# Kernel tuning notes

Measured on AMD Instinct MI355X. Metric: run time of the kernel, lower is better.

Reference implementation:

```python
import jax, jax.numpy as jnp
import numpy as np

# Model dims (ViT-Base @ 384)
L, H, D, HD, M, P, IMG, B, NC, CH = 12, 12, 768, 64, 3072, 16, 384, 32, 1000, 3
NPATCH = (IMG // P) ** 2  # 576
SCALE = 1.0 / np.sqrt(HD)


def setup_inputs() -> dict:
    key = jax.random.key(0)
    ks = iter(jax.random.split(key, 16))
    def n(shape, s=0.02):
        return (jax.random.normal(next(ks), shape, jnp.float32) * s).astype(jnp.float32)
    return dict(
        x=jax.random.normal(next(ks), (B, CH, IMG, IMG), jnp.float32),
        conv_w=n((D, CH, P, P)), conv_b=jnp.zeros((D,), jnp.float32),
        cls_token=jnp.zeros((1, 1, D), jnp.float32),
        pos_emb=n((1, NPATCH + 1, D), 1.0),
        ln1_g=jnp.ones((L, D), jnp.float32), ln1_b=jnp.zeros((L, D), jnp.float32),
        wqkv=n((L, H, D, 3 * HD)), bqkv=jnp.zeros((L, H, 3 * HD), jnp.float32),
        wmsa=n((L, D, D)), bmsa=jnp.zeros((L, D), jnp.float32),
        ln2_g=jnp.ones((L, D), jnp.float32), ln2_b=jnp.zeros((L, D), jnp.float32),
        lnm_g=jnp.ones((L, D), jnp.float32), lnm_b=jnp.zeros((L, D), jnp.float32),
        w1=n((L, D, M)), b1=jnp.zeros((L, M), jnp.float32),
        w2=n((L, M, D)), b2=jnp.zeros((L, D), jnp.float32),
        lnf_g=jnp.ones((D,), jnp.float32), lnf_b=jnp.zeros((D,), jnp.float32),
        whead=n((D, NC)), bhead=jnp.zeros((NC,), jnp.float32),
    )


def _ln(x, g, b, eps=1e-5):
    mu = jnp.mean(x, axis=-1, keepdims=True)
    var = jnp.mean(jnp.square(x - mu), axis=-1, keepdims=True)
    return (x - mu) * jax.lax.rsqrt(var + eps) * g + b


def _encoder_block(x, p):
    (ln1_g, ln1_b, wqkv, bqkv, wmsa, bmsa,
     ln2_g, ln2_b, lnm_g, lnm_b, w1, b1, w2, b2) = p
    b = x.shape[0]
    h = _ln(x, ln1_g, ln1_b)
    # batched per-head QKV (math identical to looping over H small Linears)
    qkv = jnp.einsum('bsd,hde->bhse', h, wqkv) + bqkv[:, None, :]  # [B,H,S,3*HD]
    q, k, v = jnp.split(qkv, 3, axis=-1)
    attn = jax.nn.softmax(jnp.einsum('bhqe,bhke->bhqk', q, k) * SCALE, axis=-1)
    o = jnp.einsum('bhqk,bhke->bhqe', attn, v)          # [B,H,S,HD]
    o = o.transpose(0, 2, 1, 3).reshape(b, -1, D)        # concat heads along feature
    msa = jnp.einsum('bsd,de->bse', o, wmsa) + bmsa
    x1 = h + msa                                          # residual around MSA (post-LN1)
    h2 = _ln(x1, ln2_g, ln2_b)
    h2 = _ln(h2, lnm_g, lnm_b)                            # MLPBlock's own LayerNorm (double LN, faithful)
    mlp = jnp.einsum('bsm,md->bsd', jax.nn.gelu(jnp.einsum('bsd,dm->bsm', h2, w1) + b1, approximate=False), w2) + b2
    return x1 + mlp, None


def reference(x, conv_w, conv_b, cls_token, pos_emb,
              ln1_g, ln1_b, wqkv, bqkv, wmsa, bmsa,
              ln2_g, ln2_b, lnm_g, lnm_b, w1, b1, w2, b2,
              lnf_g, lnf_b, whead, bhead):
    b = x.shape[0]
    # patchify conv (image divisible by patch, so F.pad is a no-op)
    t = jax.lax.conv_general_dilated(x, conv_w, (P, P), 'VALID',
                                     dimension_numbers=('NCHW', 'OIHW', 'NCHW'))
    t = t + conv_b[None, :, None, None]
    # faithful to torch .view(b, -1, embed_dim) on NCHW layout (channel-major flatten)
    t = t.reshape(b, -1, D)
    n = t.shape[1]
    t = jnp.concatenate([jnp.broadcast_to(cls_token, (b, 1, D)), t], axis=1)
    t = t + pos_emb[:, :n + 1]
    stacked = (ln1_g, ln1_b, wqkv, bqkv, wmsa, bmsa,
               ln2_g, ln2_b, lnm_g, lnm_b, w1, b1, w2, b2)
    t, _ = jax.lax.scan(_encoder_block, t, stacked)
    y = _ln(t[:, 0], lnf_g, lnf_b)
    y = jax.nn.softmax(jnp.einsum('bd,dc->bc', y, whead) + bhead, axis=-1)
    return y
```

## Files before the change

### kernel.cpp

```cpp
#include <hip/hip_runtime.h>

using f16   = _Float16;
using f16x8 = __attribute__((ext_vector_type(8))) _Float16;
using f32x4 = __attribute__((ext_vector_type(4))) float;

#define MPAD  18560
#define MREAL 18464
#define MCONV 18432
#define SEQ   577
#define SPAD  640
#define NHEAD 12
#define NBATCH 32
#define SC2   0.18033688f
#define THR2  11.5416f

__device__ __forceinline__ void load_lds16(const void* g, void* l) {
  __builtin_amdgcn_global_load_lds(
      (const __attribute__((address_space(1))) void*)g,
      (__attribute__((address_space(3))) void*)l, 16, 0, 0);
}

template<int K, int EPI>
__global__ __launch_bounds__(256) void gemm_k(
    const f16* __restrict__ A, const f16* __restrict__ Bt,
    const float* __restrict__ bias, const float* __restrict__ res,
    float* __restrict__ o32, f16* __restrict__ o16a, f16* __restrict__ o16b,
    f16* __restrict__ o16c, const float* __restrict__ pos,
    const float* __restrict__ lng, const float* __restrict__ lnb,
    const float* __restrict__ stats, int N, int Mreal)
{
  static_assert(K % 64 == 0, "BK=64");
  __shared__ __align__(16) f16 As[128 * 64];
  __shared__ __align__(16) f16 Bs[128 * 64];
  const int tid = threadIdx.x;
  const int lane = tid & 63, wv = tid >> 6;

  const int gx = gridDim.x, gy = gridDim.y;
  const int nwg = gx * gy;
  const int flat = blockIdx.y * gx + blockIdx.x;
  const int xcd = flat & 7;
  const int qq = nwg >> 3, rr = nwg & 7;
  const int p_ = ((xcd < rr) ? xcd * (qq + 1) : rr * (qq + 1) + (xcd - rr) * qq)
                 + (flat >> 3);
  const int bandsz = gy * 6;
  const int band = p_ / bandsz, within = p_ - band * bandsz;
  const int byi = within / 6;
  const int bxi = band * 6 + (within - byi * 6);
  const int bm = byi << 7, bn = bxi << 7;

  const int wm = (wv >> 1) << 6, wn = (wv & 1) << 6;
  const int r16 = lane & 15, g4 = lane >> 4;
  const f32x4 Z4 = {0.f, 0.f, 0.f, 0.f};

  f32x4 acc[4][4];
#pragma unroll
  for (int m = 0; m < 4; ++m)
#pragma unroll
    for (int n = 0; n < 4; ++n) acc[m][n] = Z4;

  const int srow = lane >> 3;
  const int sgc  = (lane & 7) ^ srow;
  const f16* Agp = A  + (size_t)(bm + srow) * K + sgc * 8;
  const f16* Bgp = Bt + (size_t)(bn + srow) * K + sgc * 8;

  for (int k0 = 0; k0 < K; k0 += 64) {
#pragma unroll
    for (int j = 0; j < 4; ++j) {
      const size_t roff = (size_t)((wv * 4 + j) * 8) * K + k0;
      load_lds16(Agp + roff, As + (wv * 4 + j) * 512);
      load_lds16(Bgp + roff, Bs + (wv * 4 + j) * 512);
    }
    __syncthreads();
#pragma unroll
    for (int ks = 0; ks < 2; ++ks) {
      f16x8 af[4], bf[4];
#pragma unroll
      for (int m = 0; m < 4; ++m) {
        int row = wm + m * 16 + r16;
        af[m] = *(const f16x8*)(As + row * 64 + ((((ks << 2) | g4) ^ (row & 7)) << 3));
      }
#pragma unroll
      for (int n = 0; n < 4; ++n) {
        int row = wn + n * 16 + r16;
        bf[n] = *(const f16x8*)(Bs + row * 64 + ((((ks << 2) | g4) ^ (row & 7)) << 3));
      }
#pragma unroll
      for (int m = 0; m < 4; ++m)
#pragma unroll
        for (int n = 0; n < 4; ++n)
          acc[m][n] = __builtin_amdgcn_mfma_f32_16x16x32_f16(af[m], bf[n], acc[m][n], 0, 0, 0);
    }
    __syncthreads();
  }

#pragma unroll
  for (int m = 0; m < 4; ++m) {
#pragma unroll
    for (int n = 0; n < 4; ++n) {
#pragma unroll
      for (int r = 0; r < 4; ++r) {
        int grow = bm + wm + m * 16 + g4 * 4 + r;
        int gcol = bn + wn + n * 16 + r16;
        float v = acc[m][n][r];
        if constexpr (EPI == 0) {
          if (grow < Mreal) {
            int b = grow / 576, p = grow - b * 576;
            int i = gcol * 576 + p;
            int sp = i / 768, dd = i - sp * 768;
            o32[((size_t)(b * SEQ + sp + 1)) * 768 + dd] =
                v + bias[gcol] + pos[(size_t)(sp + 1) * 768 + dd];
          }
        } else if constexpr (EPI == 1) {
          if (grow < Mreal) {
            int b = grow / SEQ, s = grow - b * SEQ;
            int hq = gcol / 192, rem = gcol - hq * 192;
            int sel = rem >> 6, e = rem & 63;
            float val = v + bias[gcol];
            int bh = b * NHEAD + hq;
            if (sel == 0)      o16a[((size_t)bh * SPAD + s) * 64 + e] = (f16)val;
            else if (sel == 1) o16b[((size_t)bh * SPAD + s) * 64 + e] = (f16)val;
            else               o16c[((size_t)bh * 64 + e) * SPAD + s] = (f16)val;
          }
        } else if constexpr (EPI == 2) {
          size_t idx = (size_t)grow * N + gcol;
          o32[idx] = v + bias[gcol] + res[idx];
        } else if constexpr (EPI == 4) {
          if (grow < Mreal) {
            size_t idx = (size_t)grow * N + gcol;
            float mu = stats[2 * grow], rs = stats[2 * grow + 1];
            float h = (res[idx] - mu) * rs * lng[gcol] + lnb[gcol];
            o32[idx] = v + bias[gcol] + h;
          }
        } else {
          float val = v + bias[gcol];
          float gl = 0.5f * val * (1.0f + erff(val * 0.70710678f));
          o16a[(size_t)grow * N + gcol] = (f16)gl;
        }
      }
    }
  }
}

__device__ __forceinline__ void block_red2(float& a, float& b, float* sm, int tid) {
  __syncthreads();
#pragma unroll
  for (int d = 32; d; d >>= 1) { a += __shfl_down(a, d); b += __shfl_down(b, d); }
  if ((tid & 63) == 0) { int w = tid >> 6; sm[w] = a; sm[w + 4] = b; }
  __syncthreads();
  a = sm[0] + sm[1] + sm[2] + sm[3];
  b = sm[4] + sm[5] + sm[6] + sm[7];
}

__global__ __launch_bounds__(256) void ln_fwd(const float* __restrict__ X,
    const float* __restrict__ g, const float* __restrict__ bb,
    float* __restrict__ stats, f16* __restrict__ hh)
{
  int row = blockIdx.x, tid = threadIdx.x;
  const float* x = X + (size_t)row * 768;
  float v0 = x[tid], v1 = x[tid + 256], v2 = x[tid + 512];
  float s = v0 + v1 + v2, s2 = v0*v0 + v1*v1 + v2*v2;
  __shared__ float sm[8];
  block_red2(s, s2, sm, tid);
  float mu = s * (1.f/768.f);
  float var = s2 * (1.f/768.f) - mu * mu;
  float rs = rsqrtf(var + 1e-5f);
  if (tid == 0) { stats[2 * row] = mu; stats[2 * row + 1] = rs; }
  size_t base = (size_t)row * 768;
  hh[base + tid      ] = (f16)((v0 - mu) * rs * g[tid      ] + bb[tid      ]);
  hh[base + tid + 256] = (f16)((v1 - mu) * rs * g[tid + 256] + bb[tid + 256]);
  hh[base + tid + 512] = (f16)((v2 - mu) * rs * g[tid + 512] + bb[tid + 512]);
}

__global__ __launch_bounds__(256) void ln2_fwd(const float* __restrict__ X,
    const float* __restrict__ g2, const float* __restrict__ bb2,
    const float* __restrict__ gm, const float* __restrict__ bbm,
    f16* __restrict__ hh)
{
  int row = blockIdx.x, tid = threadIdx.x;
  const float* x = X + (size_t)row * 768;
  float v0 = x[tid], v1 = x[tid + 256], v2 = x[tid + 512];
  float s = v0 + v1 + v2, s2 = v0*v0 + v1*v1 + v2*v2;
  __shared__ float sm[8];
  block_red2(s, s2, sm, tid);
  float mu = s * (1.f/768.f), var = s2 * (1.f/768.f) - mu * mu;
  float rs = rsqrtf(var + 1e-5f);
  float y0 = (v0 - mu) * rs * g2[tid      ] + bb2[tid      ];
  float y1 = (v1 - mu) * rs * g2[tid + 256] + bb2[tid + 256];
  float y2 = (v2 - mu) * rs * g2[tid + 512] + bb2[tid + 512];
  s = y0 + y1 + y2; s2 = y0*y0 + y1*y1 + y2*y2;
  block_red2(s, s2, sm, tid);
  mu = s * (1.f/768.f); var = s2 * (1.f/768.f) - mu * mu;
  rs = rsqrtf(var + 1e-5f);
  size_t base = (size_t)row * 768;
  hh[base + tid      ] = (f16)((y0 - mu) * rs * gm[tid      ] + bbm[tid      ]);
  hh[base + tid + 256] = (f16)((y1 - mu) * rs * gm[tid + 256] + bbm[tid + 256]);
  hh[base + tid + 512] = (f16)((y2 - mu) * rs * gm[tid + 512] + bbm[tid + 512]);
}

__global__ __launch_bounds__(256) void attn_k(const f16* __restrict__ qbuf,
    const f16* __restrict__ kbuf, const f16* __restrict__ vtbuf,
    f16* __restrict__ obuf)
{
  const int gx = gridDim.x;
  const int nwg = gx * gridDim.y;
  const int flat = blockIdx.y * gx + blockIdx.x;
  const int xcd = flat & 7;
  const int qq = nwg >> 3, rr = nwg & 7;
  const int pos_ = ((xcd < rr) ? xcd * (qq + 1) : rr * (qq + 1) + (xcd - rr) * qq)
                   + (flat >> 3);
  const int bh = pos_ / gx;
  const int s0 = (pos_ - bh * gx) << 6;

  const int b = bh / NHEAD, hd = bh - b * NHEAD;
  const int tid = threadIdx.x, lane = tid & 63, wv = tid >> 6;
  const int r16 = lane & 15, g4 = lane >> 4;
  const f16* Q  = qbuf  + (size_t)bh * SPAD * 64;
  const f16* Kg = kbuf  + (size_t)bh * SPAD * 64;
  const f16* Vg = vtbuf + (size_t)bh * 64 * SPAD;
  __shared__ __align__(16) f16 Kt[64 * 64];
  __shared__ __align__(16) f16 Vt[64 * 64];
  __shared__ __align__(16) f16 Pw[4][16][72];
  const f32x4 Z4 = {0.f, 0.f, 0.f, 0.f};

  f16x8 qf[2];
  {
    const f16* qr = Q + (size_t)(s0 + wv * 16 + r16) * 64;
    qf[0] = *(const f16x8*)(qr + g4 * 8);
    qf[1] = *(const f16x8*)(qr + 32 + g4 * 8);
  }
  float m_run[4] = {-1e30f, -1e30f, -1e30f, -1e30f};
  float l_part[4] = {0.f, 0.f, 0.f, 0.f};
  f32x4 o_acc[4];
#pragma unroll
  for (int n = 0; n < 4; ++n) o_acc[n] = Z4;

  auto tile = [&](int kt, bool mask) {
#pragma unroll
    for (int j = 0; j < 2; ++j) {
      int off = (wv * 2 + j) * 1024 + lane * 16;
      int row = off >> 7;
      int cs  = (off >> 4) & 7;
      int gc  = cs ^ (row & 7);
      load_lds16(Kg + (size_t)(kt + row) * 64 + gc * 8, (void*)((char*)Kt + (wv*2 + j) * 1024));
      load_lds16(Vg + (size_t)row * SPAD + kt + gc * 8, (void*)((char*)Vt + (wv*2 + j) * 1024));
    }
    __syncthreads();

    f32x4 sa[4];
#pragma unroll
    for (int n = 0; n < 4; ++n) sa[n] = Z4;
#pragma unroll
    for (int n = 0; n < 4; ++n) {
      int krow = n * 16 + r16;
#pragma unroll
      for (int kc = 0; kc < 2; ++kc) {
        f16x8 kf = *(const f16x8*)(Kt + krow * 64 + (((kc * 4 + g4) ^ (krow & 7)) << 3));
        sa[n] = __builtin_amdgcn_mfma_f32_16x16x32_f16(qf[kc], kf, sa[n], 0, 0, 0);
      }
    }
#pragma unroll
    for (int r = 0; r < 4; ++r) {
      float mx = -1e30f;
#pragma unroll
      for (int n = 0; n < 4; ++n) {
        float sv = sa[n][r] * SC2;
        if (mask && (kt + n * 16 + r16 >= SEQ)) sv = -1e30f;
        sa[n][r] = sv;
        mx = fmaxf(mx, sv);
      }
#pragma unroll
      for (int d = 1; d < 16; d <<= 1) mx = fmaxf(mx, __shfl_xor(mx, d));
      if (!__all(mx - m_run[r] <= THR2)) {
        float mnew = fmaxf(m_run[r], mx);
        float alpha = exp2f(m_run[r] - mnew);
        m_run[r] = mnew;
        l_part[r] *= alpha;
#pragma unroll
        for (int n = 0; n < 4; ++n) o_acc[n][r] *= alpha;
      }
#pragma unroll
      for (int n = 0; n < 4; ++n) {
        float p = exp2f(sa[n][r] - m_run[r]);
        l_part[r] += p;
        Pw[wv][g4 * 4 + r][n * 16 + r16] = (f16)p;
      }
    }
    f16x8 pf[2];
    pf[0] = *(const f16x8*)(&Pw[wv][r16][g4 * 8]);
    pf[1] = *(const f16x8*)(&Pw[wv][r16][32 + g4 * 8]);
#pragma unroll
    for (int n = 0; n < 4; ++n) {
      int erow = n * 16 + r16;
#pragma unroll
      for (int kc = 0; kc < 2; ++kc) {
        f16x8 vf = *(const f16x8*)(Vt + erow * 64 + (((kc * 4 + g4) ^ (erow & 7)) << 3));
        o_acc[n] = __builtin_amdgcn_mfma_f32_16x16x32_f16(pf[kc], vf, o_acc[n], 0, 0, 0);
      }
    }
    __syncthreads();
  };

#pragma unroll 1
  for (int kt = 0; kt < 576; kt += 64) tile(kt, false);
  tile(576, true);

  float inv[4];
#pragma unroll
  for (int r = 0; r < 4; ++r) {
    float l = l_part[r];
#pragma unroll
    for (int d = 1; d < 16; d <<= 1) l += __shfl_xor(l, d);
    inv[r] = 1.f / l;
  }
#pragma unroll
  for (int n = 0; n < 4; ++n)
#pragma unroll
    for (int r = 0; r < 4; ++r) {
      int s = s0 + wv * 16 + g4 * 4 + r;
      if (s < SEQ)
        obuf[((size_t)(b * SEQ + s)) * 768 + hd * 64 + n * 16 + r16] =
            (f16)(o_acc[n][r] * inv[r]);
    }
}

__global__ __launch_bounds__(256) void cvt_transpose(const float* __restrict__ in,
    f16* __restrict__ out, int K, int N, size_t ls_in, size_t ls_out)
{
  in  += (size_t)blockIdx.z * ls_in;
  out += (size_t)blockIdx.z * ls_out;
  __shared__ float t[32][33];
  int n0 = blockIdx.x << 5, k0 = blockIdx.y << 5;
  int tx = threadIdx.x & 31, ty = threadIdx.x >> 5;
#pragma unroll
  for (int i = 0; i < 4; ++i) t[ty + 8*i][tx] = in[(size_t)(k0 + ty + 8*i) * N + n0 + tx];
  __syncthreads();
#pragma unroll
  for (int i = 0; i < 4; ++i) out[(size_t)(n0 + ty + 8*i) * K + k0 + tx] = (f16)t[tx][ty + 8*i];
}

__global__ __launch_bounds__(256) void cvt_qkvw(const float* __restrict__ in,
    f16* __restrict__ out, size_t ls_in, size_t ls_out)
{
  in  += (size_t)blockIdx.z * ls_in;
  out += (size_t)blockIdx.z * ls_out;
  __shared__ float t[32][33];
  int n0 = blockIdx.x << 5, k0 = blockIdx.y << 5;
  int tx = threadIdx.x & 31, ty = threadIdx.x >> 5;
  int hq = n0 / 192, r0 = n0 - hq * 192;
#pragma unroll
  for (int i = 0; i < 4; ++i)
    t[ty + 8*i][tx] = in[(size_t)hq * 147456 + (size_t)(k0 + ty + 8*i) * 192 + r0 + tx];
  __syncthreads();
#pragma unroll
  for (int i = 0; i < 4; ++i) out[(size_t)(n0 + ty + 8*i) * 768 + k0 + tx] = (f16)t[tx][ty + 8*i];
}

__global__ __launch_bounds__(256) void cvt_plain(const float* __restrict__ in,
    f16* __restrict__ out, int n)
{
  int i = blockIdx.x * 1024 + threadIdx.x;
#pragma unroll
  for (int j = 0; j < 4; ++j) { int idx = i + j * 256; if (idx < n) out[idx] = (f16)in[idx]; }
}

__global__ __launch_bounds__(256) void zero_vpad(f16* __restrict__ vtb) {
  int bh = blockIdx.x;
  for (int idx = threadIdx.x; idx < 64 * (SPAD - SEQ); idx += 256) {
    int e = idx / (SPAD - SEQ), s = SEQ + idx - e * (SPAD - SEQ);
    vtb[((size_t)bh * 64 + e) * SPAD + s] = (f16)0.f;
  }
}

__global__ __launch_bounds__(256) void im2col_k(const float* __restrict__ x, f16* __restrict__ out) {
  int row = blockIdx.x;
  int b = row / 576, p = row - b * 576;
  int py = p / 24, px = p - py * 24;
  int tid = threadIdx.x;
#pragma unroll
  for (int j = 0; j < 3; ++j) {
    int k = tid + j * 256;
    int c = k >> 8, rem = k & 255;
    int iy = rem >> 4, ix = rem & 15;
    out[(size_t)row * 768 + k] =
        (f16)x[(((size_t)(b * 3 + c)) * 384 + py * 16 + iy) * 384 + px * 16 + ix];
  }
}

__global__ __launch_bounds__(256) void cls_k(const float* __restrict__ ct,
    const float* __restrict__ pos, float* __restrict__ X)
{
  int b = blockIdx.x, tid = threadIdx.x;
#pragma unroll
  for (int j = 0; j < 3; ++j) {
    int d0 = tid + j * 256;
    X[((size_t)b * SEQ) * 768 + d0] = ct[d0] + pos[d0];
  }
}

__global__ __launch_bounds__(256) void head_logits(const float* __restrict__ X,
    const float* __restrict__ g, const float* __restrict__ bb,
    const float* __restrict__ W, const float* __restrict__ bhd,
    float* __restrict__ lg)
{
  int b = blockIdx.x, tid = threadIdx.x;
  const float* x = X + (size_t)(b * SEQ) * 768;
  float v0 = x[tid], v1 = x[tid + 256], v2 = x[tid + 512];
  float s = v0 + v1 + v2, s2 = v0*v0 + v1*v1 + v2*v2;
  __shared__ float sm[8];
  block_red2(s, s2, sm, tid);
  float mu = s * (1.f/768.f), var = s2 * (1.f/768.f) - mu * mu;
  float rs = rsqrtf(var + 1e-5f);
  __shared__ float y[768];
  y[tid      ] = (v0 - mu) * rs * g[tid      ] + bb[tid      ];
  y[tid + 256] = (v1 - mu) * rs * g[tid + 256] + bb[tid + 256];
  y[tid + 512] = (v2 - mu) * rs * g[tid + 512] + bb[tid + 512];
  __syncthreads();
  int c = blockIdx.y * 250 + tid;
  if (tid < 250) {
    float a0 = 0.f, a1 = 0.f, a2 = 0.f, a3 = 0.f;
#pragma unroll 4
    for (int d = 0; d < 768; d += 4) {
      a0 = fmaf(y[d    ], W[(size_t)(d    ) * 1000 + c], a0);
      a1 = fmaf(y[d + 1], W[(size_t)(d + 1) * 1000 + c], a1);
      a2 = fmaf(y[d + 2], W[(size_t)(d + 2) * 1000 + c], a2);
      a3 = fmaf(y[d + 3], W[(size_t)(d + 3) * 1000 + c], a3);
    }
    lg[(size_t)b * 1000 + c] = (a0 + a1) + (a2 + a3) + bhd[c];
  }
}

__global__ __launch_bounds__(256) void head_soft(const float* __restrict__ lg,
    float* __restrict__ out)
{
  int b = blockIdx.x, tid = threadIdx.x;
  __shared__ float sm[8];
  float v[4], mx = -1e30f;
#pragma unroll
  for (int j = 0; j < 4; ++j) {
    int c = tid + j * 256;
    v[j] = (c < 1000) ? lg[(size_t)b * 1000 + c] : -1e30f;
    mx = fmaxf(mx, v[j]);
  }
#pragma unroll
  for (int d = 32; d; d >>= 1) mx = fmaxf(mx, __shfl_down(mx, d));
  if ((tid & 63) == 0) sm[tid >> 6] = mx;
  __syncthreads();
  mx = fmaxf(fmaxf(sm[0], sm[1]), fmaxf(sm[2], sm[3]));
  float se = 0.f, ex[4];
#pragma unroll
  for (int j = 0; j < 4; ++j) {
    int c = tid + j * 256;
    ex[j] = (c < 1000) ? __expf(v[j] - mx) : 0.f;
    se += ex[j];
  }
  __syncthreads();
#pragma unroll
  for (int d = 32; d; d >>= 1) se += __shfl_down(se, d);
  if ((tid & 63) == 0) sm[tid >> 6] = se;
  __syncthreads();
  se = sm[0] + sm[1] + sm[2] + sm[3];
  float inv = 1.f / se;
#pragma unroll
  for (int j = 0; j < 4; ++j) {
    int c = tid + j * 256;
    if (c < 1000) out[(size_t)b * 1000 + c] = ex[j] * inv;
  }
}

extern "C" void kernel_launch(void* const* d_in, const int* in_sizes, int n_in,
                              void* d_out, int out_size, void* d_ws, size_t ws_size,
                              hipStream_t stream)
{
  (void)in_sizes; (void)n_in; (void)out_size;
  const float* x      = (const float*)d_in[0];
  const float* conv_w = (const float*)d_in[1];
  const float* conv_b = (const float*)d_in[2];
  const float* cls_t  = (const float*)d_in[3];
  const float* pos    = (const float*)d_in[4];
  const float* ln1_g  = (const float*)d_in[5];
  const float* ln1_b  = (const float*)d_in[6];
  const float* wqkv   = (const float*)d_in[7];
  const float* bqkv   = (const float*)d_in[8];
  const float* wmsa   = (const float*)d_in[9];
  const float* bmsa   = (const float*)d_in[10];
  const float* ln2_g  = (const float*)d_in[11];
  const float* ln2_b  = (const float*)d_in[12];
  const float* lnm_g  = (const float*)d_in[13];
  const float* lnm_b  = (const float*)d_in[14];
  const float* w1     = (const float*)d_in[15];
  const float* b1     = (const float*)d_in[16];
  const float* w2     = (const float*)d_in[17];
  const float* b2     = (const float*)d_in[18];
  const float* lnf_g  = (const float*)d_in[19];
  const float* lnf_b  = (const float*)d_in[20];
  const float* whead  = (const float*)d_in[21];
  const float* bhead  = (const float*)d_in[22];
  float* out = (float*)d_out;

  const size_t szQ  = (size_t)2304 * 768;
  const size_t szM  = (size_t)768 * 768;
  const size_t szW1 = (size_t)3072 * 768;
  const size_t szW2 = (size_t)768 * 3072;
  const size_t fixed_bytes =
      (size_t)MPAD * 768 * 4 + (size_t)MPAD * 8 + 32 * 1000 * 4 +
      (size_t)MPAD * 768 * 2 +
      (size_t)MPAD * 3072 * 2 + 3 * ((size_t)NBATCH * NHEAD * SPAD * 64 * 2) +
      (size_t)768 * 768 * 2  + 16 * 256 ;
  const bool hoist =
      ws_size >= fixed_bytes + 12 * (szQ + szM + szW1 + szW2) * 2 + 8 * 256;
  const int LW = hoist ? 12 : 1;

  char* wsp = (char*)d_ws;
  size_t off = 0;
  auto alloc = [&](size_t bytes) {
    char* p = wsp + off; off += (bytes + 255) & ~(size_t)255; return p;
  };
  float* X    = (float*)alloc((size_t)MPAD * 768 * 4);
  float* stats= (float*)alloc((size_t)MPAD * 8);
  float* lgbuf= (float*)alloc((size_t)32 * 1000 * 4);
  f16*   hh   = (f16*)  alloc((size_t)MPAD * 768 * 2);
  f16*   abuf = (f16*)  alloc((size_t)MPAD * 3072 * 2);
  f16*   qb   = (f16*)  alloc((size_t)NBATCH * NHEAD * SPAD * 64 * 2);
  f16*   kb   = (f16*)  alloc((size_t)NBATCH * NHEAD * SPAD * 64 * 2);
  f16*   vtb  = (f16*)  alloc((size_t)NBATCH * NHEAD * SPAD * 64 * 2);
  f16*   WcT  = (f16*)  alloc((size_t)768 * 768 * 2);
  f16*   WqkvT= (f16*)  alloc(LW * szQ  * 2);
  f16*   WmsaT= (f16*)  alloc(LW * szM  * 2);
  f16*   W1T  = (f16*)  alloc(LW * szW1 * 2);
  f16*   W2T  = (f16*)  alloc(LW * szW2 * 2);
  f16*   obuf   = abuf;
  f16*   patchA = abuf;
  f16*   h2h    = hh;
  if (ws_size < off) return;

  zero_vpad<<<dim3(NBATCH * NHEAD), 256, 0, stream>>>(vtb);
  cvt_plain<<<dim3((768 * 768 + 1023) / 1024), 256, 0, stream>>>(conv_w, WcT, 768 * 768);
  if (hoist) {
    cvt_qkvw<<<dim3(72, 24, 12), 256, 0, stream>>>(wqkv, WqkvT, (size_t)12*768*192, szQ);
    cvt_transpose<<<dim3(24, 24, 12), 256, 0, stream>>>(wmsa, WmsaT, 768, 768, szM, szM);
    cvt_transpose<<<dim3(96, 24, 12), 256, 0, stream>>>(w1, W1T, 768, 3072, szW1, szW1);
    cvt_transpose<<<dim3(24, 96, 12), 256, 0, stream>>>(w2, W2T, 3072, 768, szW2, szW2);
  }
  im2col_k<<<dim3(MCONV), 256, 0, stream>>>(x, patchA);
  gemm_k<768, 0><<<dim3(6, 144), 256, 0, stream>>>(
      patchA, WcT, conv_b, nullptr, X, nullptr, nullptr, nullptr, pos,
      nullptr, nullptr, nullptr, 768, MCONV);
  cls_k<<<dim3(NBATCH), 256, 0, stream>>>(cls_t, pos, X);

  for (int l = 0; l < 12; ++l) {
    f16* wq  = WqkvT + (hoist ? (size_t)l * szQ  : 0);
    f16* wms = WmsaT + (hoist ? (size_t)l * szM  : 0);
    f16* w1t = W1T   + (hoist ? (size_t)l * szW1 : 0);
    f16* w2t = W2T   + (hoist ? (size_t)l * szW2 : 0);
    if (!hoist) {
      cvt_qkvw<<<dim3(72, 24), 256, 0, stream>>>(
          wqkv + (size_t)l * 12 * 768 * 192, wq, 0, 0);
      cvt_transpose<<<dim3(24, 24), 256, 0, stream>>>(
          wmsa + (size_t)l * 768 * 768, wms, 768, 768, 0, 0);
      cvt_transpose<<<dim3(96, 24), 256, 0, stream>>>(
          w1 + (size_t)l * 768 * 3072, w1t, 768, 3072, 0, 0);
      cvt_transpose<<<dim3(24, 96), 256, 0, stream>>>(
          w2 + (size_t)l * 3072 * 768, w2t, 3072, 768, 0, 0);
    }

    ln_fwd<<<dim3(MREAL), 256, 0, stream>>>(X, ln1_g + l * 768, ln1_b + l * 768, stats, hh);
    gemm_k<768, 1><<<dim3(18, 145), 256, 0, stream>>>(
        hh, wq, bqkv + (size_t)l * 2304, nullptr, nullptr, qb, kb, vtb, nullptr,
        nullptr, nullptr, nullptr, 2304, MREAL);
    attn_k<<<dim3(10, NBATCH * NHEAD), 256, 0, stream>>>(qb, kb, vtb, obuf);
    gemm_k<768, 4><<<dim3(6, 145), 256, 0, stream>>>(
        obuf, wms, bmsa + l * 768, X, X, nullptr, nullptr, nullptr, nullptr,
        ln1_g + l * 768, ln1_b + l * 768, stats, 768, MREAL);
    ln2_fwd<<<dim3(MREAL), 256, 0, stream>>>(
        X, ln2_g + l * 768, ln2_b + l * 768, lnm_g + l * 768, lnm_b + l * 768, h2h);
    gemm_k<768, 3><<<dim3(24, 145), 256, 0, stream>>>(
        h2h, w1t, b1 + (size_t)l * 3072, nullptr, nullptr, abuf, nullptr, nullptr, nullptr,
        nullptr, nullptr, nullptr, 3072, MREAL);
    gemm_k<3072, 2><<<dim3(6, 145), 256, 0, stream>>>(
        abuf, w2t, b2 + l * 768, X, X, nullptr, nullptr, nullptr, nullptr,
        nullptr, nullptr, nullptr, 768, MREAL);
  }
  head_logits<<<dim3(NBATCH, 4), 256, 0, stream>>>(X, lnf_g, lnf_b, whead, bhead, lgbuf);
  head_soft<<<dim3(NBATCH), 256, 0, stream>>>(lgbuf, out);
}
```

Before: 7.831 ms.

## Process two query tiles per attention block and hoist GEMM LDS offsets

```diff
diff --git a/kernel.cpp b/kernel.cpp
--- a/kernel.cpp
+++ b/kernel.cpp
@@ -63,6 +63,19 @@
   const f16* Agp = A  + (size_t)(bm + srow) * K + sgc * 8;
   const f16* Bgp = Bt + (size_t)(bn + srow) * K + sgc * 8;
 
+  int aoff[2][4], boff[2][4];
+#pragma unroll
+  for (int ks = 0; ks < 2; ++ks) {
+#pragma unroll
+    for (int m = 0; m < 4; ++m) {
+      int arow = wm + m * 16 + r16;
+      aoff[ks][m] = arow * 64 + ((((ks << 2) | g4) ^ (arow & 7)) << 3);
+      int brow = wn + m * 16 + r16;
+      boff[ks][m] = brow * 64 + ((((ks << 2) | g4) ^ (brow & 7)) << 3);
+    }
+  }
+
+#pragma unroll 2
   for (int k0 = 0; k0 < K; k0 += 64) {
 #pragma unroll
     for (int j = 0; j < 4; ++j) {
@@ -75,15 +88,9 @@
     for (int ks = 0; ks < 2; ++ks) {
       f16x8 af[4], bf[4];
 #pragma unroll
-      for (int m = 0; m < 4; ++m) {
-        int row = wm + m * 16 + r16;
-        af[m] = *(const f16x8*)(As + row * 64 + ((((ks << 2) | g4) ^ (row & 7)) << 3));
-      }
-#pragma unroll
-      for (int n = 0; n < 4; ++n) {
-        int row = wn + n * 16 + r16;
-        bf[n] = *(const f16x8*)(Bs + row * 64 + ((((ks << 2) | g4) ^ (row & 7)) << 3));
-      }
+      for (int m = 0; m < 4; ++m) af[m] = *(const f16x8*)(As + aoff[ks][m]);
+#pragma unroll
+      for (int n = 0; n < 4; ++n) bf[n] = *(const f16x8*)(Bs + boff[ks][n]);
 #pragma unroll
       for (int m = 0; m < 4; ++m)
 #pragma unroll
@@ -209,7 +216,7 @@
   const int pos_ = ((xcd < rr) ? xcd * (qq + 1) : rr * (qq + 1) + (xcd - rr) * qq)
                    + (flat >> 3);
   const int bh = pos_ / gx;
-  const int s0 = (pos_ - bh * gx) << 6;
+  const int q0 = (pos_ - bh * gx) << 7;
 
   const int b = bh / NHEAD, hd = bh - b * NHEAD;
   const int tid = threadIdx.x, lane = tid & 63, wv = tid >> 6;
@@ -222,17 +229,21 @@
   __shared__ __align__(16) f16 Pw[4][16][72];
   const f32x4 Z4 = {0.f, 0.f, 0.f, 0.f};
 
-  f16x8 qf[2];
-  {
-    const f16* qr = Q + (size_t)(s0 + wv * 16 + r16) * 64;
-    qf[0] = *(const f16x8*)(qr + g4 * 8);
-    qf[1] = *(const f16x8*)(qr + 32 + g4 * 8);
-  }
-  float m_run[4] = {-1e30f, -1e30f, -1e30f, -1e30f};
-  float l_part[4] = {0.f, 0.f, 0.f, 0.f};
-  f32x4 o_acc[4];
-#pragma unroll
-  for (int n = 0; n < 4; ++n) o_acc[n] = Z4;
+  f16x8 qf[2][2];
+#pragma unroll
+  for (int h = 0; h < 2; ++h) {
+    const f16* qr = Q + (size_t)(q0 + h * 64 + wv * 16 + r16) * 64;
+    qf[h][0] = *(const f16x8*)(qr + g4 * 8);
+    qf[h][1] = *(const f16x8*)(qr + 32 + g4 * 8);
+  }
+  float m_run[2][4], l_part[2][4];
+  f32x4 o_acc[2][4];
+#pragma unroll
+  for (int h = 0; h < 2; ++h)
+#pragma unroll
+    for (int n = 0; n < 4; ++n) {
+      m_run[h][n] = -1e30f; l_part[h][n] = 0.f; o_acc[h][n] = Z4;
+    }
 
   auto tile = [&](int kt, bool mask) {
 #pragma unroll
@@ -246,55 +257,58 @@
     }
     __syncthreads();
 
-    f32x4 sa[4];
-#pragma unroll
-    for (int n = 0; n < 4; ++n) sa[n] = Z4;
-#pragma unroll
-    for (int n = 0; n < 4; ++n) {
-      int krow = n * 16 + r16;
-#pragma unroll
-      for (int kc = 0; kc < 2; ++kc) {
-        f16x8 kf = *(const f16x8*)(Kt + krow * 64 + (((kc * 4 + g4) ^ (krow & 7)) << 3));
-        sa[n] = __builtin_amdgcn_mfma_f32_16x16x32_f16(qf[kc], kf, sa[n], 0, 0, 0);
+#pragma unroll
+    for (int h = 0; h < 2; ++h) {
+      f32x4 sa[4];
+#pragma unroll
+      for (int n = 0; n < 4; ++n) sa[n] = Z4;
+#pragma unroll
+      for (int n = 0; n < 4; ++n) {
+        int krow = n * 16 + r16;
+#pragma unroll
+        for (int kc = 0; kc < 2; ++kc) {
+          f16x8 kf = *(const f16x8*)(Kt + krow * 64 + (((kc * 4 + g4) ^ (krow & 7)) << 3));
+          sa[n] = __builtin_amdgcn_mfma_f32_16x16x32_f16(qf[h][kc], kf, sa[n], 0, 0, 0);
+        }
       }
-    }
-#pragma unroll
-    for (int r = 0; r < 4; ++r) {
-      float mx = -1e30f;
+#pragma unroll
+      for (int r = 0; r < 4; ++r) {
+        float mx = -1e30f;
+#pragma unroll
+        for (int n = 0; n < 4; ++n) {
+          float sv = sa[n][r] * SC2;
+          if (mask && (kt + n * 16 + r16 >= SEQ)) sv = -1e30f;
+          sa[n][r] = sv;
+          mx = fmaxf(mx, sv);
+        }
+#pragma unroll
+        for (int d = 1; d < 16; d <<= 1) mx = fmaxf(mx, __shfl_xor(mx, d));
+        if (!__all(mx - m_run[h][r] <= THR2)) {
+          float mnew = fmaxf(m_run[h][r], mx);
+          float alpha = exp2f(m_run[h][r] - mnew);
+          m_run[h][r] = mnew;
+          l_part[h][r] *= alpha;
+#pragma unroll
+          for (int n = 0; n < 4; ++n) o_acc[h][n][r] *= alpha;
+        }
+#pragma unroll
+        for (int n = 0; n < 4; ++n) {
+          float p = exp2f(sa[n][r] - m_run[h][r]);
+          l_part[h][r] += p;
+          Pw[wv][g4 * 4 + r][n * 16 + r16] = (f16)p;
+        }
+      }
+      f16x8 pf[2];
+      pf[0] = *(const f16x8*)(&Pw[wv][r16][g4 * 8]);
+      pf[1] = *(const f16x8*)(&Pw[wv][r16][32 + g4 * 8]);
 #pragma unroll
       for (int n = 0; n < 4; ++n) {
-        float sv = sa[n][r] * SC2;
-        if (mask && (kt + n * 16 + r16 >= SEQ)) sv = -1e30f;
-        sa[n][r] = sv;
-        mx = fmaxf(mx, sv);
-      }
-#pragma unroll
-      for (int d = 1; d < 16; d <<= 1) mx = fmaxf(mx, __shfl_xor(mx, d));
-      if (!__all(mx - m_run[r] <= THR2)) {
-        float mnew = fmaxf(m_run[r], mx);
-        float alpha = exp2f(m_run[r] - mnew);
-        m_run[r] = mnew;
-        l_part[r] *= alpha;
-#pragma unroll
-        for (int n = 0; n < 4; ++n) o_acc[n][r] *= alpha;
-      }
-#pragma unroll
-      for (int n = 0; n < 4; ++n) {
-        float p = exp2f(sa[n][r] - m_run[r]);
-        l_part[r] += p;
-        Pw[wv][g4 * 4 + r][n * 16 + r16] = (f16)p;
-      }
-    }
-    f16x8 pf[2];
-    pf[0] = *(const f16x8*)(&Pw[wv][r16][g4 * 8]);
-    pf[1] = *(const f16x8*)(&Pw[wv][r16][32 + g4 * 8]);
-#pragma unroll
-    for (int n = 0; n < 4; ++n) {
-      int erow = n * 16 + r16;
-#pragma unroll
-      for (int kc = 0; kc < 2; ++kc) {
-        f16x8 vf = *(const f16x8*)(Vt + erow * 64 + (((kc * 4 + g4) ^ (erow & 7)) << 3));
-        o_acc[n] = __builtin_amdgcn_mfma_f32_16x16x32_f16(pf[kc], vf, o_acc[n], 0, 0, 0);
+        int erow = n * 16 + r16;
+#pragma unroll
+        for (int kc = 0; kc < 2; ++kc) {
+          f16x8 vf = *(const f16x8*)(Vt + erow * 64 + (((kc * 4 + g4) ^ (erow & 7)) << 3));
+          o_acc[h][n] = __builtin_amdgcn_mfma_f32_16x16x32_f16(pf[kc], vf, o_acc[h][n], 0, 0, 0);
+        }
       }
     }
     __syncthreads();
@@ -304,23 +318,26 @@
   for (int kt = 0; kt < 576; kt += 64) tile(kt, false);
   tile(576, true);
 
-  float inv[4];
-#pragma unroll
-  for (int r = 0; r < 4; ++r) {
-    float l = l_part[r];
-#pragma unroll
-    for (int d = 1; d < 16; d <<= 1) l += __shfl_xor(l, d);
-    inv[r] = 1.f / l;
-  }
-#pragma unroll
-  for (int n = 0; n < 4; ++n)
+#pragma unroll
+  for (int h = 0; h < 2; ++h) {
+    float inv[4];
 #pragma unroll
     for (int r = 0; r < 4; ++r) {
-      int s = s0 + wv * 16 + g4 * 4 + r;
-      if (s < SEQ)
-        obuf[((size_t)(b * SEQ + s)) * 768 + hd * 64 + n * 16 + r16] =
-            (f16)(o_acc[n][r] * inv[r]);
-    }
+      float l = l_part[h][r];
+#pragma unroll
+      for (int d = 1; d < 16; d <<= 1) l += __shfl_xor(l, d);
+      inv[r] = 1.f / l;
+    }
+#pragma unroll
+    for (int n = 0; n < 4; ++n)
+#pragma unroll
+      for (int r = 0; r < 4; ++r) {
+        int s = q0 + h * 64 + wv * 16 + g4 * 4 + r;
+        if (s < SEQ)
+          obuf[((size_t)(b * SEQ + s)) * 768 + hd * 64 + n * 16 + r16] =
+              (f16)(o_acc[h][n][r] * inv[r]);
+      }
+  }
 }
 
 __global__ __launch_bounds__(256) void cvt_transpose(const float* __restrict__ in,
@@ -567,7 +584,7 @@
     gemm_k<768, 1><<<dim3(18, 145), 256, 0, stream>>>(
         hh, wq, bqkv + (size_t)l * 2304, nullptr, nullptr, qb, kb, vtb, nullptr,
         nullptr, nullptr, nullptr, 2304, MREAL);
-    attn_k<<<dim3(10, NBATCH * NHEAD), 256, 0, stream>>>(qb, kb, vtb, obuf);
+    attn_k<<<dim3(5, NBATCH * NHEAD), 256, 0, stream>>>(qb, kb, vtb, obuf);
     gemm_k<768, 4><<<dim3(6, 145), 256, 0, stream>>>(
         obuf, wms, bmsa + l * 768, X, X, nullptr, nullptr, nullptr, nullptr,
         ln1_g + l * 768, ln1_b + l * 768, stats, 768, MREAL);
```

Result: slower. 8.704 ms (+11.1%).

## Rewrite GEMM as 256x256 tile, 512-thread double-buffered pipelined kernel

Applied to the files above, without the earlier changes.

```diff
diff --git a/kernel.cpp b/kernel.cpp
--- a/kernel.cpp
+++ b/kernel.cpp
@@ -4,7 +4,7 @@
 using f16x8 = __attribute__((ext_vector_type(8))) _Float16;
 using f32x4 = __attribute__((ext_vector_type(4))) float;
 
-#define MPAD  18560
+#define MPAD2 18688
 #define MREAL 18464
 #define MCONV 18432
 #define SEQ   577
@@ -20,8 +20,11 @@
       (__attribute__((address_space(3))) void*)l, 16, 0, 0);
 }
 
+#define VMW(n) asm volatile("s_waitcnt vmcnt(" #n ")" ::: "memory")
+#define BARR() do { __builtin_amdgcn_s_barrier(); asm volatile("" ::: "memory"); } while (0)
+
 template<int K, int EPI>
-__global__ __launch_bounds__(256) void gemm_k(
+__global__ __launch_bounds__(512) void gemm_k(
     const f16* __restrict__ A, const f16* __restrict__ Bt,
     const float* __restrict__ bias, const float* __restrict__ res,
     float* __restrict__ o32, f16* __restrict__ o16a, f16* __restrict__ o16b,
@@ -30,107 +33,139 @@
     const float* __restrict__ stats, int N, int Mreal)
 {
   static_assert(K % 64 == 0, "BK=64");
-  __shared__ __align__(16) f16 As[128 * 64];
-  __shared__ __align__(16) f16 Bs[128 * 64];
+  constexpr int NT = K / 64;
+  __shared__ __align__(16) f16 As[2][256 * 64];
+  __shared__ __align__(16) f16 Bs[2][256 * 64];
   const int tid = threadIdx.x;
   const int lane = tid & 63, wv = tid >> 6;
 
-  const int gx = gridDim.x, gy = gridDim.y;
-  const int nwg = gx * gy;
+  const int gx = gridDim.x;
+  const int nwg = gx * gridDim.y;
   const int flat = blockIdx.y * gx + blockIdx.x;
   const int xcd = flat & 7;
   const int qq = nwg >> 3, rr = nwg & 7;
   const int p_ = ((xcd < rr) ? xcd * (qq + 1) : rr * (qq + 1) + (xcd - rr) * qq)
                  + (flat >> 3);
-  const int bandsz = gy * 6;
-  const int band = p_ / bandsz, within = p_ - band * bandsz;
-  const int byi = within / 6;
-  const int bxi = band * 6 + (within - byi * 6);
-  const int bm = byi << 7, bn = bxi << 7;
-
-  const int wm = (wv >> 1) << 6, wn = (wv & 1) << 6;
+  const int byi = p_ / gx, bxi = p_ - byi * gx;
+  const int bm = byi << 8, bn = bxi << 8;
+
+  const int wm = (wv >> 2) << 7;
+  const int wn = (wv & 3) << 6;
   const int r16 = lane & 15, g4 = lane >> 4;
   const f32x4 Z4 = {0.f, 0.f, 0.f, 0.f};
 
-  f32x4 acc[4][4];
-#pragma unroll
-  for (int m = 0; m < 4; ++m)
+  f32x4 acc[8][4];
+#pragma unroll
+  for (int m = 0; m < 8; ++m)
 #pragma unroll
     for (int n = 0; n < 4; ++n) acc[m][n] = Z4;
 
-  const int srow = lane >> 3;
-  const int sgc  = (lane & 7) ^ srow;
-  const f16* Agp = A  + (size_t)(bm + srow) * K + sgc * 8;
-  const f16* Bgp = Bt + (size_t)(bn + srow) * K + sgc * 8;
-
-  for (int k0 = 0; k0 < K; k0 += 64) {
-#pragma unroll
-    for (int j = 0; j < 4; ++j) {
-      const size_t roff = (size_t)((wv * 4 + j) * 8) * K + k0;
-      load_lds16(Agp + roff, As + (wv * 4 + j) * 512);
-      load_lds16(Bgp + roff, Bs + (wv * 4 + j) * 512);
-    }
-    __syncthreads();
-#pragma unroll
-    for (int ks = 0; ks < 2; ++ks) {
-      f16x8 af[4], bf[4];
-#pragma unroll
-      for (int m = 0; m < 4; ++m) {
-        int row = wm + m * 16 + r16;
-        af[m] = *(const f16x8*)(As + row * 64 + ((((ks << 2) | g4) ^ (row & 7)) << 3));
-      }
-#pragma unroll
-      for (int n = 0; n < 4; ++n) {
-        int row = wn + n * 16 + r16;
-        bf[n] = *(const f16x8*)(Bs + row * 64 + ((((ks << 2) | g4) ^ (row & 7)) << 3));
-      }
-#pragma unroll
-      for (int m = 0; m < 4; ++m)
-#pragma unroll
-        for (int n = 0; n < 4; ++n)
-          acc[m][n] = __builtin_amdgcn_mfma_f32_16x16x32_f16(af[m], bf[n], acc[m][n], 0, 0, 0);
-    }
-    __syncthreads();
-  }
-
-#pragma unroll
-  for (int m = 0; m < 4; ++m) {
-#pragma unroll
-    for (int n = 0; n < 4; ++n) {
+  const int srow8 = tid >> 3;
+  const int sgc   = (tid & 7) ^ (srow8 & 7);
+  const f16* Agp = A  + (size_t)(bm + srow8) * K + sgc * 8;
+  const f16* Bgp = Bt + (size_t)(bn + srow8) * K + sgc * 8;
+  const int ldso = (wv << 3) * 64;
+
+  auto stA = [&](f16* dst, int j, int k0) {
+    load_lds16(Agp + (size_t)(j * 64) * K + k0, dst + j * 64 * 64 + ldso);
+  };
+  auto stB = [&](f16* dst, int j, int k0) {
+    load_lds16(Bgp + (size_t)(j * 64) * K + k0, dst + j * 64 * 64 + ldso);
+  };
+  auto rdA = [&](const f16* buf, int mf, int ks) {
+    int row = wm + mf * 16 + r16;
+    return *(const f16x8*)(buf + row * 64 + ((((ks << 2) | g4) ^ (row & 7)) << 3));
+  };
+  auto rdB = [&](const f16* buf, int nf, int ks) {
+    int row = wn + nf * 16 + r16;
+    return *(const f16x8*)(buf + row * 64 + ((((ks << 2) | g4) ^ (row & 7)) << 3));
+  };
+
+  stB(Bs[0], 0, 0); stB(Bs[0], 1, 0); stB(Bs[0], 2, 0); stB(Bs[0], 3, 0);
+  stA(As[0], 0, 0); stA(As[0], 2, 0); stA(As[0], 1, 0); stA(As[0], 3, 0);
+  VMW(2);
+  BARR();
+
+#pragma unroll 1
+  for (int t = 0; t < NT; ++t) {
+    const f16* Ac = As[t & 1];
+    const f16* Bc = Bs[t & 1];
+    f16* An = As[(t + 1) & 1];
+    f16* Bn = Bs[(t + 1) & 1];
+    const bool pf = (t + 1 < NT);
+    const int k1 = (t + 1) << 6;
+
+    f16x8 bf[4][2];
+#pragma unroll
+    for (int nf = 0; nf < 4; ++nf) {
+      bf[nf][0] = rdB(Bc, nf, 0);
+      bf[nf][1] = rdB(Bc, nf, 1);
+    }
+    if (pf) { stB(Bn, 0, k1); stB(Bn, 1, k1); stB(Bn, 2, k1); stB(Bn, 3, k1); }
+    __builtin_amdgcn_s_setprio(1);
+#pragma unroll
+    for (int mf = 0; mf < 4; ++mf) {
+      f16x8 a0 = rdA(Ac, mf, 0), a1 = rdA(Ac, mf, 1);
+#pragma unroll
+      for (int nf = 0; nf < 4; ++nf) {
+        acc[mf][nf] = __builtin_amdgcn_mfma_f32_16x16x32_f16(a0, bf[nf][0], acc[mf][nf], 0, 0, 0);
+        acc[mf][nf] = __builtin_amdgcn_mfma_f32_16x16x32_f16(a1, bf[nf][1], acc[mf][nf], 0, 0, 0);
+      }
+    }
+    __builtin_amdgcn_s_setprio(0);
+    if (pf) VMW(4); else VMW(0);
+    BARR();
+    if (pf) { stA(An, 0, k1); stA(An, 2, k1); stA(An, 1, k1); stA(An, 3, k1); }
+    __builtin_amdgcn_s_setprio(1);
+#pragma unroll
+    for (int mf = 4; mf < 8; ++mf) {
+      f16x8 a0 = rdA(Ac, mf, 0), a1 = rdA(Ac, mf, 1);
+#pragma unroll
+      for (int nf = 0; nf < 4; ++nf) {
+        acc[mf][nf] = __builtin_amdgcn_mfma_f32_16x16x32_f16(a0, bf[nf][0], acc[mf][nf], 0, 0, 0);
+        acc[mf][nf] = __builtin_amdgcn_mfma_f32_16x16x32_f16(a1, bf[nf][1], acc[mf][nf], 0, 0, 0);
+      }
+    }
+    __builtin_amdgcn_s_setprio(0);
+    if (pf) {
+      VMW(2);
+      BARR();
+    }
+  }
+
+#pragma unroll
+  for (int mf = 0; mf < 8; ++mf) {
+#pragma unroll
+    for (int nf = 0; nf < 4; ++nf) {
 #pragma unroll
       for (int r = 0; r < 4; ++r) {
-        int grow = bm + wm + m * 16 + g4 * 4 + r;
-        int gcol = bn + wn + n * 16 + r16;
-        float v = acc[m][n][r];
+        int grow = bm + wm + mf * 16 + g4 * 4 + r;
+        int gcol = bn + wn + nf * 16 + r16;
+        if (grow >= Mreal) continue;
+        float v = acc[mf][nf][r];
         if constexpr (EPI == 0) {
-          if (grow < Mreal) {
-            int b = grow / 576, p = grow - b * 576;
-            int i = gcol * 576 + p;
-            int sp = i / 768, dd = i - sp * 768;
-            o32[((size_t)(b * SEQ + sp + 1)) * 768 + dd] =
-                v + bias[gcol] + pos[(size_t)(sp + 1) * 768 + dd];
-          }
+          int b = grow / 576, p = grow - b * 576;
+          int i = gcol * 576 + p;
+          int sp = i / 768, dd = i - sp * 768;
+          o32[((size_t)(b * SEQ + sp + 1)) * 768 + dd] =
+              v + bias[gcol] + pos[(size_t)(sp + 1) * 768 + dd];
         } else if constexpr (EPI == 1) {
-          if (grow < Mreal) {
-            int b = grow / SEQ, s = grow - b * SEQ;
-            int hq = gcol / 192, rem = gcol - hq * 192;
-            int sel = rem >> 6, e = rem & 63;
-            float val = v + bias[gcol];
-            int bh = b * NHEAD + hq;
-            if (sel == 0)      o16a[((size_t)bh * SPAD + s) * 64 + e] = (f16)val;
-            else if (sel == 1) o16b[((size_t)bh * SPAD + s) * 64 + e] = (f16)val;
-            else               o16c[((size_t)bh * 64 + e) * SPAD + s] = (f16)val;
-          }
+          int b = grow / SEQ, s = grow - b * SEQ;
+          int hq = gcol / 192, rem = gcol - hq * 192;
+          int sel = rem >> 6, e = rem & 63;
+          float val = v + bias[gcol];
+          int bh = b * NHEAD + hq;
+          if (sel == 0)      o16a[((size_t)bh * SPAD + s) * 64 + e] = (f16)val;
+          else if (sel == 1) o16b[((size_t)bh * SPAD + s) * 64 + e] = (f16)val;
+          else               o16c[((size_t)bh * 64 + e) * SPAD + s] = (f16)val;
         } else if constexpr (EPI == 2) {
           size_t idx = (size_t)grow * N + gcol;
           o32[idx] = v + bias[gcol] + res[idx];
         } else if constexpr (EPI == 4) {
-          if (grow < Mreal) {
-            size_t idx = (size_t)grow * N + gcol;
-            float mu = stats[2 * grow], rs = stats[2 * grow + 1];
-            float h = (res[idx] - mu) * rs * lng[gcol] + lnb[gcol];
-            o32[idx] = v + bias[gcol] + h;
-          }
+          size_t idx = (size_t)grow * N + gcol;
+          float mu = stats[2 * grow], rs = stats[2 * grow + 1];
+          float h = (res[idx] - mu) * rs * lng[gcol] + lnb[gcol];
+          o32[idx] = v + bias[gcol] + h;
         } else {
           float val = v + bias[gcol];
           float gl = 0.5f * val * (1.0f + erff(val * 0.70710678f));
@@ -502,9 +537,9 @@
   const size_t szW1 = (size_t)3072 * 768;
   const size_t szW2 = (size_t)768 * 3072;
   const size_t fixed_bytes =
-      (size_t)MPAD * 768 * 4 + (size_t)MPAD * 8 + 32 * 1000 * 4 +
-      (size_t)MPAD * 768 * 2 +
-      (size_t)MPAD * 3072 * 2 + 3 * ((size_t)NBATCH * NHEAD * SPAD * 64 * 2) +
+      (size_t)MPAD2 * 768 * 4 + (size_t)MPAD2 * 8 + 32 * 1000 * 4 +
+      (size_t)MPAD2 * 768 * 2 +
+      (size_t)MPAD2 * 3072 * 2 + 3 * ((size_t)NBATCH * NHEAD * SPAD * 64 * 2) +
       (size_t)768 * 768 * 2  + 16 * 256 ;
   const bool hoist =
       ws_size >= fixed_bytes + 12 * (szQ + szM + szW1 + szW2) * 2 + 8 * 256;
@@ -515,11 +550,11 @@
   auto alloc = [&](size_t bytes) {
     char* p = wsp + off; off += (bytes + 255) & ~(size_t)255; return p;
   };
-  float* X    = (float*)alloc((size_t)MPAD * 768 * 4);
-  float* stats= (float*)alloc((size_t)MPAD * 8);
+  float* X    = (float*)alloc((size_t)MPAD2 * 768 * 4);
+  float* stats= (float*)alloc((size_t)MPAD2 * 8);
   float* lgbuf= (float*)alloc((size_t)32 * 1000 * 4);
-  f16*   hh   = (f16*)  alloc((size_t)MPAD * 768 * 2);
-  f16*   abuf = (f16*)  alloc((size_t)MPAD * 3072 * 2);
+  f16*   hh   = (f16*)  alloc((size_t)MPAD2 * 768 * 2);
+  f16*   abuf = (f16*)  alloc((size_t)MPAD2 * 3072 * 2);
   f16*   qb   = (f16*)  alloc((size_t)NBATCH * NHEAD * SPAD * 64 * 2);
   f16*   kb   = (f16*)  alloc((size_t)NBATCH * NHEAD * SPAD * 64 * 2);
   f16*   vtb  = (f16*)  alloc((size_t)NBATCH * NHEAD * SPAD * 64 * 2);
@@ -542,7 +577,7 @@
     cvt_transpose<<<dim3(24, 96, 12), 256, 0, stream>>>(w2, W2T, 3072, 768, szW2, szW2);
   }
   im2col_k<<<dim3(MCONV), 256, 0, stream>>>(x, patchA);
-  gemm_k<768, 0><<<dim3(6, 144), 256, 0, stream>>>(
+  gemm_k<768, 0><<<dim3(3, 72), 512, 0, stream>>>(
       patchA, WcT, conv_b, nullptr, X, nullptr, nullptr, nullptr, pos,
       nullptr, nullptr, nullptr, 768, MCONV);
   cls_k<<<dim3(NBATCH), 256, 0, stream>>>(cls_t, pos, X);
@@ -564,19 +599,19 @@
     }
 
     ln_fwd<<<dim3(MREAL), 256, 0, stream>>>(X, ln1_g + l * 768, ln1_b + l * 768, stats, hh);
-    gemm_k<768, 1><<<dim3(18, 145), 256, 0, stream>>>(
+    gemm_k<768, 1><<<dim3(9, 73), 512, 0, stream>>>(
         hh, wq, bqkv + (size_t)l * 2304, nullptr, nullptr, qb, kb, vtb, nullptr,
         nullptr, nullptr, nullptr, 2304, MREAL);
     attn_k<<<dim3(10, NBATCH * NHEAD), 256, 0, stream>>>(qb, kb, vtb, obuf);
-    gemm_k<768, 4><<<dim3(6, 145), 256, 0, stream>>>(
+    gemm_k<768, 4><<<dim3(3, 73), 512, 0, stream>>>(
         obuf, wms, bmsa + l * 768, X, X, nullptr, nullptr, nullptr, nullptr,
         ln1_g + l * 768, ln1_b + l * 768, stats, 768, MREAL);
     ln2_fwd<<<dim3(MREAL), 256, 0, stream>>>(
         X, ln2_g + l * 768, ln2_b + l * 768, lnm_g + l * 768, lnm_b + l * 768, h2h);
-    gemm_k<768, 3><<<dim3(24, 145), 256, 0, stream>>>(
+    gemm_k<768, 3><<<dim3(12, 73), 512, 0, stream>>>(
         h2h, w1t, b1 + (size_t)l * 3072, nullptr, nullptr, abuf, nullptr, nullptr, nullptr,
         nullptr, nullptr, nullptr, 3072, MREAL);
-    gemm_k<3072, 2><<<dim3(6, 145), 256, 0, stream>>>(
+    gemm_k<3072, 2><<<dim3(3, 73), 512, 0, stream>>>(
         abuf, w2t, b2 + l * 768, X, X, nullptr, nullptr, nullptr, nullptr,
         nullptr, nullptr, nullptr, 768, MREAL);
   }
```

After: 9.092 ms. 1.16x slower.
